# Performance work log

Measured on AMD Instinct MI355X. Metric: run time of the kernel, lower is better.

## Reference

```python
import jax, jax.numpy as jnp
import numpy as np

NUM_GRAPHS = 256
T, F_IN, F_OUT, D_E = 5, 75, 15, 50   # towers, per-tower in, per-tower out, edge emb dim
N_LAYERS = 4
AVG_DEG_LOG = float(np.log(17.0))     # from deg histogram: all nodes have degree 16 -> mean log(deg+1)=log(17)
BN_EPS = 1e-5
STD_EPS = 1e-5


def _pna_conv(h, src, dst, e_enc, pw, pb, qw, qb, lw, lb):
    """One PNAConv layer (divide_input=False, pre_layers=post_layers=1)."""
    N = h.shape[0]
    x_i, x_j = h[dst], h[src]                      # gather target/source node feats [E, F_IN]
    # pre-NN Linear(3*F_IN -> F_IN) per tower, applied to cat([x_i, x_j, e_enc]); split the weight
    Wi, Wj, We = pw[:, :F_IN], pw[:, F_IN:2 * F_IN], pw[:, 2 * F_IN:]
    m = (jnp.einsum('ef,tfg->etg', x_i, Wi)
         + jnp.einsum('ef,tfg->etg', x_j, Wj)
         + jnp.einsum('ef,tfg->etg', e_enc, We) + pb)   # [E, T, F_IN]
    ones = jnp.ones((m.shape[0],), h.dtype)
    cnt = jax.ops.segment_sum(ones, dst, N)        # in-degree per node
    deg = jnp.maximum(cnt, 1.0)[:, None, None]
    mean = jax.ops.segment_sum(m, dst, N) / deg
    mean2 = jax.ops.segment_sum(m * m, dst, N) / deg
    std = jnp.sqrt(jax.nn.relu(mean2 - mean * mean) + STD_EPS)
    has_edge = (cnt > 0)[:, None, None]
    mn = jnp.where(has_edge, jax.ops.segment_min(m, dst, N), 0.0)
    mx = jnp.where(has_edge, jax.ops.segment_max(m, dst, N), 0.0)
    agg = jnp.concatenate([mean, mn, mx, std], axis=-1)          # [N, T, 4*F_IN]
    amp = (jnp.log(jnp.maximum(cnt, 1.0) + 1.0) / AVG_DEG_LOG)[:, None, None]
    out = jnp.concatenate([agg, agg * amp, agg / amp], axis=-1)  # identity/amplification/attenuation [N,T,12*F_IN]
    post = jnp.einsum('ntf,tfg->ntg', out, qw) + qb              # post-NN Linear(900 -> 15) per tower
    return post.reshape(N, T * F_OUT) @ lw + lb                  # mixing Linear(75 -> 75)


def setup_inputs() -> dict:
    key = jax.random.key(0)
    ks = iter(jax.random.split(key, 64))
    N, E = 16384, 262144
    g = lambda shape, s=0.1: jax.random.normal(next(ks), shape, jnp.float32) * s
    return dict(
        x=jax.random.randint(next(ks), (N,), 0, 21),
        edge_index=jax.random.randint(next(ks), (2, E), 0, N),
        edge_attr=jax.random.randint(next(ks), (E,), 0, 4),
        batch=jnp.sort(jax.random.randint(next(ks), (N,), 0, NUM_GRAPHS)),
        node_emb=g((21, F_IN)),
        edge_emb=g((4, D_E)),
        edge_enc_w=g((N_LAYERS, D_E, F_IN)), edge_enc_b=jnp.zeros((N_LAYERS, F_IN)),
        pre_w=g((N_LAYERS, T, 3 * F_IN, F_IN)), pre_b=jnp.zeros((N_LAYERS, T, F_IN)),
        post_w=g((N_LAYERS, T, 12 * F_IN, F_OUT)), post_b=jnp.zeros((N_LAYERS, T, F_OUT)),
        lin_w=g((N_LAYERS, T * F_OUT, T * F_OUT)), lin_b=jnp.zeros((N_LAYERS, T * F_OUT)),
        bn_gamma=jnp.ones((N_LAYERS, 75)), bn_beta=jnp.zeros((N_LAYERS, 75)),
        mlp_w1=g((75, 50)), mlp_b1=jnp.zeros((50,)),
        mlp_w2=g((50, 25)), mlp_b2=jnp.zeros((25,)),
        mlp_w3=g((25, 1)), mlp_b3=jnp.zeros((1,)),
    )


def reference(x, edge_index, edge_attr, batch, node_emb, edge_emb,
              edge_enc_w, edge_enc_b, pre_w, pre_b, post_w, post_b,
              lin_w, lin_b, bn_gamma, bn_beta,
              mlp_w1, mlp_b1, mlp_w2, mlp_b2, mlp_w3, mlp_b3):
    h = node_emb[x]                    # [N, 75]
    e = edge_emb[edge_attr]            # [E, 50]
    src, dst = edge_index[0], edge_index[1]
    for l in range(N_LAYERS):
        e_enc = e @ edge_enc_w[l] + edge_enc_b[l]   # edge encoder Linear(50->75)
        h = _pna_conv(h, src, dst, e_enc, pre_w[l], pre_b[l],
                      post_w[l], post_b[l], lin_w[l], lin_b[l])
        mu = h.mean(0)
        var = ((h - mu) ** 2).mean(0)               # biased batch-norm variance (training mode)
        h = jax.nn.relu((h - mu) / jnp.sqrt(var + BN_EPS) * bn_gamma[l] + bn_beta[l])
    g = jax.ops.segment_sum(h, batch, NUM_GRAPHS)   # global_add_pool [G, 75]
    g = jax.nn.relu(g @ mlp_w1 + mlp_b1)
    g = jax.nn.relu(g @ mlp_w2 + mlp_b2)
    return g @ mlp_w3 + mlp_b3                      # [G, 1]
```

## Files before the change

### kernel.cpp

```cpp
#include <hip/hip_runtime.h>
#include <math.h>

#define N_NODES 16384
#define N_EDGES 262144
#define TOW 5
#define FI 75
#define FO 15
#define DE 50
#define NL 4
#define NG 256
#define HWP 752
#define ATS 16400
#define ENB 8

static __device__ __attribute__((aligned(16))) float g_hA[N_NODES*FI];
static __device__ __attribute__((aligned(16))) float g_hB[N_NODES*FI];
static __device__ __attribute__((aligned(16))) float g_hW[N_NODES*HWP];
static __device__ __attribute__((aligned(16))) float g_ec[NL*4*376];
static __device__ __attribute__((aligned(16))) float g_qwP[NL*TOW*3*300*16];
static __device__ int    g_deg[N_NODES];
static __device__ int    g_rowstart[N_NODES+1];
static __device__ int    g_cursor[N_NODES];
static __device__ int    g_edge[N_EDGES];
static __device__ double g_bns1[FI];
static __device__ double g_bns2[FI];
static __device__ float  g_pool[NG*FI];

__global__ void k_embed(const int* __restrict__ x, const float* __restrict__ node_emb) {
    int i = blockIdx.x * blockDim.x + threadIdx.x;
    if (i < N_NODES*FI) {
        int n = i / FI, f = i % FI;
        g_hA[i] = node_emb[x[n]*FI + f];
    }
}

__global__ void k_zerodeg() {
    int i = blockIdx.x * blockDim.x + threadIdx.x;
    if (i < N_NODES) g_deg[i] = 0;
}

__global__ void k_hist(const int* __restrict__ dst) {
    int e = blockIdx.x * blockDim.x + threadIdx.x;
    if (e < N_EDGES) atomicAdd(&g_deg[dst[e]], 1);
}

__global__ void k_scan() {
    __shared__ int part[1024];
    int t = threadIdx.x;
    int base = t * 16;
    int loc[16];
    int s = 0;
    #pragma unroll
    for (int i = 0; i < 16; i++) { loc[i] = s; s += g_deg[base + i]; }
    part[t] = s;
    __syncthreads();
    for (int off = 1; off < 1024; off <<= 1) {
        int v = 0;
        if (t >= off) v = part[t - off];
        __syncthreads();
        if (t >= off) part[t] += v;
        __syncthreads();
    }
    int excl = (t == 0) ? 0 : part[t - 1];
    #pragma unroll
    for (int i = 0; i < 16; i++) {
        g_rowstart[base + i] = excl + loc[i];
        g_cursor[base + i]   = excl + loc[i];
    }
    if (t == 1023) g_rowstart[N_NODES] = part[1023];
}

__global__ void k_scatter(const int* __restrict__ src, const int* __restrict__ dst,
                          const int* __restrict__ attr) {
    int e = blockIdx.x * blockDim.x + threadIdx.x;
    if (e < N_EDGES) {
        int d = dst[e];
        int pos = atomicAdd(&g_cursor[d], 1);
        g_edge[pos] = src[e] | (attr[e] << 16);
    }
}

__global__ void k_wq(const float* __restrict__ post_w) {
    int i = blockIdx.x * blockDim.x + threadIdx.x;
    if (i < NL*TOW*900*FO) {
        int g = i % FO;
        int r = i / FO;
        int f = r % 900;
        int lt = r / 900;
        int s = f / 300, k = f % 300;
        g_qwP[((lt*3 + s)*300 + k)*16 + g] = post_w[i];
    }
}

__global__ void k_ec(const float* __restrict__ edge_emb, const float* __restrict__ edge_enc_w,
                     const float* __restrict__ edge_enc_b, const float* __restrict__ pre_w,
                     const float* __restrict__ pre_b) {
    int l = blockIdx.x;
    const float* eew = edge_enc_w + l*DE*FI;
    const float* eeb = edge_enc_b + l*FI;
    const float* pw  = pre_w + l*TOW*3*FI*FI;
    const float* pb  = pre_b + l*TOW*FI;
    __shared__ float e_enc[4*FI];
    int t = threadIdx.x;
    if (t < 4*FI) {
        int a = t / FI, f = t % FI;
        float s = eeb[f];
        for (int d = 0; d < DE; d++) s += edge_emb[a*DE + d] * eew[d*FI + f];
        e_enc[t] = s;
    }
    __syncthreads();
    for (int o = t; o < 4*376; o += blockDim.x) {
        int a = o / 376;
        int r = o % 376;
        float s = 0.f;
        if (r < TOW*FI) {
            int tw = r / FI, g = r % FI;
            s = pb[tw*FI + g];
            const float* W = pw + (tw*(3*FI) + 2*FI)*FI + g;
            for (int f = 0; f < FI; f++) s += e_enc[a*FI + f] * W[f*FI];
        }
        g_ec[l*1504 + o] = s;
    }
}

#define NPB 8
__global__ void k_hw(const float* __restrict__ pw, const float* __restrict__ gamma,
                     const float* __restrict__ beta, int first) {
    __shared__ float hsh[NPB*FI];
    int n0 = blockIdx.x * NPB;
    int tid = threadIdx.x;
    for (int i = tid; i < NPB*FI; i += blockDim.x) {
        int idx = (n0 + i/FI)*FI + (i % FI);
        float v;
        if (first) {
            v = g_hA[idx];
        } else {
            int c = i % FI;
            double mud  = g_bns1[c] * (1.0/N_NODES);
            double vard = g_bns2[c] * (1.0/N_NODES) - mud*mud;
            if (vard < 0.0) vard = 0.0;
            float mu   = (float)mud;
            float rsig = (float)(1.0 / sqrt(vard + 1e-5));
            v = (g_hB[idx] - mu) * rsig * gamma[c] + beta[c];
            v = v > 0.f ? v : 0.f;
        }
        hsh[i] = v;
    }
    __syncthreads();
    for (int o = tid; o < 2*TOW*FI; o += blockDim.x) {
        int half = o / (TOW*FI);
        int r = o % (TOW*FI);
        int tw = r / FI, g = r % FI;
        const float* W = pw + (tw*(3*FI) + half*FI)*FI + g;
        float acc[NPB];
        #pragma unroll
        for (int nn = 0; nn < NPB; nn++) acc[nn] = 0.f;
        for (int f = 0; f < FI; f++) {
            float w = W[f*FI];
            #pragma unroll
            for (int nn = 0; nn < NPB; nn++) acc[nn] += hsh[nn*FI + f] * w;
        }
        #pragma unroll
        for (int nn = 0; nn < NPB; nn++)
            g_hW[(n0+nn)*HWP + half*376 + r] = acc[nn];
    }
}

__global__ __launch_bounds__(128*ENB) void k_edge(int l, float* __restrict__ aggT) {
    __shared__ float aggl[ENB][1504];
    int tid = threadIdx.x;
    if (blockIdx.x == 0 && tid < FI) { g_bns1[tid] = 0.0; g_bns2[tid] = 0.0; }
    int wp  = tid >> 7;
    int q   = tid & 127;
    int n   = blockIdx.x * ENB + wp;
    bool act = q < 94;
    const float* ec = g_ec + l*1504;
    int e0 = g_rowstart[n], e1 = g_rowstart[n+1];
    int cnt = e1 - e0;

    float s0=0.f,s1=0.f,s2=0.f,s3=0.f;
    float t0=0.f,t1=0.f,t2=0.f,t3=0.f;
    float mn0=1e30f,mn1=1e30f,mn2=1e30f,mn3=1e30f;
    float mx0=-1e30f,mx1=-1e30f,mx2=-1e30f,mx3=-1e30f;
    float h0=0.f,h1=0.f,h2=0.f,h3=0.f;
    if (act) {
        float4 hv = *(const float4*)&g_hW[n*HWP + 4*q];
        h0=hv.x; h1=hv.y; h2=hv.z; h3=hv.w;
    }

    for (int e = e0; e < e1; e += 4) {
        int i1 = e+1, i2 = e+2, i3 = e+3;
        int pk0 = g_edge[e];
        int pk1 = g_edge[i1 < e1 ? i1 : e];
        int pk2 = g_edge[i2 < e1 ? i2 : e];
        int pk3 = g_edge[i3 < e1 ? i3 : e];
        if (act) {
            float4 hj0 = *(const float4*)&g_hW[(pk0 & 0xFFFF)*HWP + 376 + 4*q];
            float4 hj1 = *(const float4*)&g_hW[(pk1 & 0xFFFF)*HWP + 376 + 4*q];
            float4 hj2 = *(const float4*)&g_hW[(pk2 & 0xFFFF)*HWP + 376 + 4*q];
            float4 hj3 = *(const float4*)&g_hW[(pk3 & 0xFFFF)*HWP + 376 + 4*q];
            float4 ev0 = *(const float4*)&ec[(pk0 >> 16)*376 + 4*q];
            float4 ev1 = *(const float4*)&ec[(pk1 >> 16)*376 + 4*q];
            float4 ev2 = *(const float4*)&ec[(pk2 >> 16)*376 + 4*q];
            float4 ev3 = *(const float4*)&ec[(pk3 >> 16)*376 + 4*q];
            #define ACCUM(ii, hj, ev)                                        \
                if (ii < e1) {                                               \
                    float m0 = h0 + hj.x + ev.x;                             \
                    float m1 = h1 + hj.y + ev.y;                             \
                    float m2 = h2 + hj.z + ev.z;                             \
                    float m3 = h3 + hj.w + ev.w;                             \
                    s0 += m0; s1 += m1; s2 += m2; s3 += m3;                  \
                    t0 += m0*m0; t1 += m1*m1; t2 += m2*m2; t3 += m3*m3;      \
                    mn0 = fminf(mn0,m0); mn1 = fminf(mn1,m1);                \
                    mn2 = fminf(mn2,m2); mn3 = fminf(mn3,m3);                \
                    mx0 = fmaxf(mx0,m0); mx1 = fmaxf(mx1,m1);                \
                    mx2 = fmaxf(mx2,m2); mx3 = fmaxf(mx3,m3);                \
                }
            ACCUM(e,  hj0, ev0)
            ACCUM(i1, hj1, ev1)
            ACCUM(i2, hj2, ev2)
            ACCUM(i3, hj3, ev3)
            #undef ACCUM
        }
    }

    if (act) {
        float inv = 1.0f / ((cnt > 0) ? (float)cnt : 1.0f);
        float sv[4]  = {s0,s1,s2,s3};
        float tv[4]  = {t0,t1,t2,t3};
        float mnv[4] = {mn0,mn1,mn2,mn3};
        float mxv[4] = {mx0,mx1,mx2,mx3};
        #pragma unroll
        for (int j = 0; j < 4; j++) {
            int c = 4*q + j;
            if (c < TOW*FI) {
                int tw = c / FI, f = c - tw*FI;
                float mean  = sv[j]*inv;
                float mean2 = tv[j]*inv;
                float var = mean2 - mean*mean;
                if (var < 0.f) var = 0.f;
                int b = tw*300 + f;
                aggl[wp][b      ] = mean;
                aggl[wp][b +  75] = (cnt > 0) ? mnv[j] : 0.f;
                aggl[wp][b + 150] = (cnt > 0) ? mxv[j] : 0.f;
                aggl[wp][b + 225] = sqrtf(var + 1e-5f);
            }
        }
    }
    __syncthreads();
    int n0 = blockIdx.x * ENB;
    for (int c = tid; c < 1500; c += 128*ENB) {
        float4 v0 = make_float4(aggl[0][c], aggl[1][c], aggl[2][c], aggl[3][c]);
        float4 v1 = make_float4(aggl[4][c], aggl[5][c], aggl[6][c], aggl[7][c]);
        *(float4*)&aggT[(size_t)c*ATS + n0]     = v0;
        *(float4*)&aggT[(size_t)c*ATS + n0 + 4] = v1;
    }
}

__global__ __launch_bounds__(960) void
k_post3(int l, const float* __restrict__ aggT, const float* __restrict__ qb,
        const float* __restrict__ lw, const float* __restrict__ lb) {
    __shared__ float part[TOW*3*FO*64];
    int lane = threadIdx.x;
    int wv   = __builtin_amdgcn_readfirstlane(threadIdx.y);
    int tw = wv / 3, kc = wv % 3;
    int n0 = blockIdx.x * 64;
    int n  = n0 + lane;

    int cnt = g_rowstart[n+1] - g_rowstart[n];
    float deg = (cnt > 0) ? (float)cnt : 1.0f;
    float amp  = logf(deg + 1.0f) * (1.0f/2.8332133440562162f);
    float iamp = 1.0f / amp;

    const float* A  = aggT + (size_t)(tw*300 + kc*100)*ATS + n0;
    int ltw = l*TOW + tw;
    const float* W0 = g_qwP + ((ltw*3 + 0)*300 + kc*100)*16;
    const float* W1 = g_qwP + ((ltw*3 + 1)*300 + kc*100)*16;
    const float* W2 = g_qwP + ((ltw*3 + 2)*300 + kc*100)*16;

    float a0[FO], a1[FO], a2[FO];
    #pragma unroll
    for (int g = 0; g < FO; g++) { a0[g]=0.f; a1[g]=0.f; a2[g]=0.f; }

    for (int k = 0; k < 100; ++k) {
        float av = A[(size_t)k*ATS + lane];
        const float4* w0 = (const float4*)(W0 + k*16);
        const float4* w1 = (const float4*)(W1 + k*16);
        const float4* w2 = (const float4*)(W2 + k*16);
        float4 q0a=w0[0], q0b=w0[1], q0c=w0[2], q0d=w0[3];
        float4 q1a=w1[0], q1b=w1[1], q1c=w1[2], q1d=w1[3];
        float4 q2a=w2[0], q2b=w2[1], q2c=w2[2], q2d=w2[3];
        a0[0]+=av*q0a.x; a0[1]+=av*q0a.y; a0[2]+=av*q0a.z; a0[3]+=av*q0a.w;
        a0[4]+=av*q0b.x; a0[5]+=av*q0b.y; a0[6]+=av*q0b.z; a0[7]+=av*q0b.w;
        a0[8]+=av*q0c.x; a0[9]+=av*q0c.y; a0[10]+=av*q0c.z; a0[11]+=av*q0c.w;
        a0[12]+=av*q0d.x; a0[13]+=av*q0d.y; a0[14]+=av*q0d.z;
        a1[0]+=av*q1a.x; a1[1]+=av*q1a.y; a1[2]+=av*q1a.z; a1[3]+=av*q1a.w;
        a1[4]+=av*q1b.x; a1[5]+=av*q1b.y; a1[6]+=av*q1b.z; a1[7]+=av*q1b.w;
        a1[8]+=av*q1c.x; a1[9]+=av*q1c.y; a1[10]+=av*q1c.z; a1[11]+=av*q1c.w;
        a1[12]+=av*q1d.x; a1[13]+=av*q1d.y; a1[14]+=av*q1d.z;
        a2[0]+=av*q2a.x; a2[1]+=av*q2a.y; a2[2]+=av*q2a.z; a2[3]+=av*q2a.w;
        a2[4]+=av*q2b.x; a2[5]+=av*q2b.y; a2[6]+=av*q2b.z; a2[7]+=av*q2b.w;
        a2[8]+=av*q2c.x; a2[9]+=av*q2c.y; a2[10]+=av*q2c.z; a2[11]+=av*q2c.w;
        a2[12]+=av*q2d.x; a2[13]+=av*q2d.y; a2[14]+=av*q2d.z;
    }

    float pc[FO];
    #pragma unroll
    for (int g = 0; g < FO; g++) {
        pc[g] = a0[g] + amp*a1[g] + iamp*a2[g];
        part[((tw*3 + kc)*FO + g)*64 + lane] = pc[g];
    }
    __syncthreads();

    if (kc == 0) {
        #pragma unroll
        for (int g = 0; g < FO; g++) {
            float v = qb[tw*FO + g] + pc[g]
                    + part[((tw*3 + 1)*FO + g)*64 + lane]
                    + part[((tw*3 + 2)*FO + g)*64 + lane];
            part[((tw*3 + 0)*FO + g)*64 + lane] = v;
        }
    }
    __syncthreads();

    float res[5];
    #pragma unroll
    for (int cc = 0; cc < 5; cc++) res[cc] = lb[wv*5 + cc];
    for (int f = 0; f < FI; f++) {
        float pv = part[((f/FO)*3*FO + (f%FO))*64 + lane];
        const float* lwf = lw + f*FI + wv*5;
        #pragma unroll
        for (int cc = 0; cc < 5; cc++) res[cc] += pv * lwf[cc];
    }

    #pragma unroll
    for (int cc = 0; cc < 5; cc++) {
        int c = wv*5 + cc;
        float v = res[cc];
        g_hB[n*FI + c] = v;
        float s = v, s2 = v*v;
        #pragma unroll
        for (int d = 1; d < 64; d <<= 1) {
            s  += __shfl_xor(s,  d);
            s2 += __shfl_xor(s2, d);
        }
        if (lane == 0) {
            atomicAdd(&g_bns1[c], (double)s);
            atomicAdd(&g_bns2[c], (double)s2);
        }
    }
}

__global__ void k_poolzero() {
    int i = blockIdx.x * blockDim.x + threadIdx.x;
    if (i < NG*FI) g_pool[i] = 0.f;
}

__global__ void k_pool(const int* __restrict__ batch, const float* __restrict__ gamma,
                       const float* __restrict__ beta) {
    int i = blockIdx.x * blockDim.x + threadIdx.x;
    if (i < N_NODES*FI) {
        int n = i / FI, c = i % FI;
        double mud  = g_bns1[c] * (1.0/N_NODES);
        double vard = g_bns2[c] * (1.0/N_NODES) - mud*mud;
        if (vard < 0.0) vard = 0.0;
        float mu   = (float)mud;
        float rsig = (float)(1.0 / sqrt(vard + 1e-5));
        float v = (g_hB[i] - mu) * rsig * gamma[c] + beta[c];
        v = v > 0.f ? v : 0.f;
        atomicAdd(&g_pool[batch[n]*FI + c], v);
    }
}

__global__ void k_mlp(const float* __restrict__ w1, const float* __restrict__ b1,
                      const float* __restrict__ w2, const float* __restrict__ b2,
                      const float* __restrict__ w3, const float* __restrict__ b3,
                      float* __restrict__ out) {
    __shared__ float gin[FI], h1[50], h2[25];
    int gi = blockIdx.x;
    int t = threadIdx.x;
    if (t < FI) gin[t] = g_pool[gi*FI + t];
    __syncthreads();
    if (t < 50) {
        float s = b1[t];
        for (int f = 0; f < FI; f++) s += gin[f] * w1[f*50 + t];
        h1[t] = s > 0.f ? s : 0.f;
    }
    __syncthreads();
    if (t < 25) {
        float s = b2[t];
        for (int f = 0; f < 50; f++) s += h1[f] * w2[f*25 + t];
        h2[t] = s > 0.f ? s : 0.f;
    }
    __syncthreads();
    if (t == 0) {
        float s = b3[0];
        for (int f = 0; f < 25; f++) s += h2[f] * w3[f];
        out[gi] = s;
    }
}

extern "C" void kernel_launch(void* const* d_in, const int* in_sizes, int n_in,
                              void* d_out, int out_size, void* d_ws, size_t ws_size,
                              hipStream_t stream) {
    const int*   x          = (const int*)  d_in[0];
    const int*   edge_index = (const int*)  d_in[1];
    const int*   edge_attr  = (const int*)  d_in[2];
    const int*   batch      = (const int*)  d_in[3];
    const float* node_emb   = (const float*)d_in[4];
    const float* edge_emb   = (const float*)d_in[5];
    const float* edge_enc_w = (const float*)d_in[6];
    const float* edge_enc_b = (const float*)d_in[7];
    const float* pre_w      = (const float*)d_in[8];
    const float* pre_b      = (const float*)d_in[9];
    const float* post_w     = (const float*)d_in[10];
    const float* post_b     = (const float*)d_in[11];
    const float* lin_w      = (const float*)d_in[12];
    const float* lin_b      = (const float*)d_in[13];
    const float* bn_gamma   = (const float*)d_in[14];
    const float* bn_beta    = (const float*)d_in[15];
    const float* mlp_w1     = (const float*)d_in[16];
    const float* mlp_b1     = (const float*)d_in[17];
    const float* mlp_w2     = (const float*)d_in[18];
    const float* mlp_b2     = (const float*)d_in[19];
    const float* mlp_w3     = (const float*)d_in[20];
    const float* mlp_b3     = (const float*)d_in[21];
    float* out  = (float*)d_out;
    float* aggT = (float*)d_ws;

    const int* src = edge_index;
    const int* dst = edge_index + N_EDGES;

    k_embed<<<(N_NODES*FI + 255)/256, 256, 0, stream>>>(x, node_emb);
    k_zerodeg<<<(N_NODES + 255)/256, 256, 0, stream>>>();
    k_hist<<<(N_EDGES + 255)/256, 256, 0, stream>>>(dst);
    k_scan<<<1, 1024, 0, stream>>>();
    k_scatter<<<(N_EDGES + 255)/256, 256, 0, stream>>>(src, dst, edge_attr);
    k_wq<<<(NL*TOW*900*FO + 255)/256, 256, 0, stream>>>(post_w);
    k_ec<<<NL, 512, 0, stream>>>(edge_emb, edge_enc_w, edge_enc_b, pre_w, pre_b);

    for (int l = 0; l < NL; l++) {
        const float* pw  = pre_w  + l*TOW*(3*FI)*FI;
        const float* qb  = post_b + l*TOW*FO;
        const float* lw  = lin_w  + l*(TOW*FO)*(TOW*FO);
        const float* lb  = lin_b  + l*TOW*FO;
        const float* gamP = bn_gamma + (l > 0 ? (l-1)*FI : 0);
        const float* betP = bn_beta  + (l > 0 ? (l-1)*FI : 0);

        k_hw<<<N_NODES/NPB, 256, 0, stream>>>(pw, gamP, betP, l == 0 ? 1 : 0);
        k_edge<<<N_NODES/ENB, 128*ENB, 0, stream>>>(l, aggT);
        k_post3<<<dim3(N_NODES/64), dim3(64,15), 0, stream>>>(l, aggT, qb, lw, lb);
    }

    k_poolzero<<<(NG*FI + 255)/256, 256, 0, stream>>>();
    k_pool<<<(N_NODES*FI + 255)/256, 256, 0, stream>>>(batch, bn_gamma + 3*FI, bn_beta + 3*FI);
    k_mlp<<<NG, 128, 0, stream>>>(mlp_w1, mlp_b1, mlp_w2, mlp_b2, mlp_w3, mlp_b3, out);
}
```

Baseline: 1.116 ms.

## Split post-NN GEMM over K into two blocks and separate mixing linear

The per-tower post-NN reduction is split along K across two grid rows (blockIdx.y), so each block does 50 K-steps instead of 100 and the grid doubles to 512 blocks. Partial sums are written to a workspace buffer, and a new kernel adds the two partials plus bias, then applies the mixing Linear and the batch-norm statistics. The aim is more parallelism and better CU occupancy for the 256-block post kernel. The cost is an extra kernel launch and a round trip of 2x75xN floats through global memory.

```diff
diff --git a/kernel.cpp b/kernel.cpp
--- a/kernel.cpp
+++ b/kernel.cpp
@@ -11,6 +11,7 @@
 #define NG 256
 #define HWP 752
 #define ATS 16400
+#define PPS 16400
 #define ENB 8
 
 static __device__ __attribute__((aligned(16))) float g_hA[N_NODES*FI];
@@ -258,12 +259,12 @@
 }
 
 __global__ __launch_bounds__(960) void
-k_post3(int l, const float* __restrict__ aggT, const float* __restrict__ qb,
-        const float* __restrict__ lw, const float* __restrict__ lb) {
-    __shared__ float part[TOW*3*FO*64];
+k_postA(int l, const float* __restrict__ aggT, float* __restrict__ postP) {
+    __shared__ float part[15*FO*64];
     int lane = threadIdx.x;
     int wv   = __builtin_amdgcn_readfirstlane(threadIdx.y);
     int tw = wv / 3, kc = wv % 3;
+    int kb = blockIdx.y;
     int n0 = blockIdx.x * 64;
     int n  = n0 + lane;
 
@@ -272,17 +273,18 @@
     float amp  = logf(deg + 1.0f) * (1.0f/2.8332133440562162f);
     float iamp = 1.0f / amp;
 
-    const float* A  = aggT + (size_t)(tw*300 + kc*100)*ATS + n0;
+    int k0 = kb*150 + kc*50;
+    const float* A  = aggT + (size_t)(tw*300 + k0)*ATS + n0;
     int ltw = l*TOW + tw;
-    const float* W0 = g_qwP + ((ltw*3 + 0)*300 + kc*100)*16;
-    const float* W1 = g_qwP + ((ltw*3 + 1)*300 + kc*100)*16;
-    const float* W2 = g_qwP + ((ltw*3 + 2)*300 + kc*100)*16;
+    const float* W0 = g_qwP + ((ltw*3 + 0)*300 + k0)*16;
+    const float* W1 = g_qwP + ((ltw*3 + 1)*300 + k0)*16;
+    const float* W2 = g_qwP + ((ltw*3 + 2)*300 + k0)*16;
 
     float a0[FO], a1[FO], a2[FO];
     #pragma unroll
     for (int g = 0; g < FO; g++) { a0[g]=0.f; a1[g]=0.f; a2[g]=0.f; }
 
-    for (int k = 0; k < 100; ++k) {
+    for (int k = 0; k < 50; ++k) {
         float av = A[(size_t)k*ATS + lane];
         const float4* w0 = (const float4*)(W0 + k*16);
         const float4* w1 = (const float4*)(W1 + k*16);
@@ -313,13 +315,31 @@
     __syncthreads();
 
     if (kc == 0) {
+        float* pp = postP + (size_t)kb*75*PPS;
         #pragma unroll
         for (int g = 0; g < FO; g++) {
-            float v = qb[tw*FO + g] + pc[g]
+            float v = pc[g]
                     + part[((tw*3 + 1)*FO + g)*64 + lane]
                     + part[((tw*3 + 2)*FO + g)*64 + lane];
-            part[((tw*3 + 0)*FO + g)*64 + lane] = v;
-        }
+            pp[(size_t)(tw*FO + g)*PPS + n] = v;
+        }
+    }
+}
+
+__global__ __launch_bounds__(960) void
+k_linB(const float* __restrict__ postP, const float* __restrict__ qb,
+       const float* __restrict__ lw, const float* __restrict__ lb) {
+    __shared__ float postl[FI*64];
+    int lane = threadIdx.x;
+    int wv   = __builtin_amdgcn_readfirstlane(threadIdx.y);
+    int n0 = blockIdx.x * 64;
+    int n  = n0 + lane;
+
+    #pragma unroll
+    for (int cc = 0; cc < 5; cc++) {
+        int c = wv*5 + cc;
+        float v = postP[(size_t)c*PPS + n] + postP[(size_t)(75 + c)*PPS + n] + qb[c];
+        postl[c*64 + lane] = v;
     }
     __syncthreads();
 
@@ -327,7 +347,7 @@
     #pragma unroll
     for (int cc = 0; cc < 5; cc++) res[cc] = lb[wv*5 + cc];
     for (int f = 0; f < FI; f++) {
-        float pv = part[((f/FO)*3*FO + (f%FO))*64 + lane];
+        float pv = postl[f*64 + lane];
         const float* lwf = lw + f*FI + wv*5;
         #pragma unroll
         for (int cc = 0; cc < 5; cc++) res[cc] += pv * lwf[cc];
@@ -425,8 +445,9 @@
     const float* mlp_b2     = (const float*)d_in[19];
     const float* mlp_w3     = (const float*)d_in[20];
     const float* mlp_b3     = (const float*)d_in[21];
-    float* out  = (float*)d_out;
-    float* aggT = (float*)d_ws;
+    float* out   = (float*)d_out;
+    float* aggT  = (float*)d_ws;
+    float* postP = aggT + (size_t)1500*ATS;
 
     const int* src = edge_index;
     const int* dst = edge_index + N_EDGES;
@@ -449,7 +470,8 @@
 
         k_hw<<<N_NODES/NPB, 256, 0, stream>>>(pw, gamP, betP, l == 0 ? 1 : 0);
         k_edge<<<N_NODES/ENB, 128*ENB, 0, stream>>>(l, aggT);
-        k_post3<<<dim3(N_NODES/64), dim3(64,15), 0, stream>>>(l, aggT, qb, lw, lb);
+        k_postA<<<dim3(N_NODES/64, 2), dim3(64,15), 0, stream>>>(l, aggT, postP);
+        k_linB<<<N_NODES/64, dim3(64,15), 0, stream>>>(postP, qb, lw, lb);
     }
 
     k_poolzero<<<(NG*FI + 255)/256, 256, 0, stream>>>();
```

New measurement: 1.145 ms. +2.6%, slower.
